# Performance work log

Measured on AMD Instinct MI355X. Metric: run time of the kernel, lower is better.

## Reference

```python
import jax, jax.numpy as jnp
import numpy as np

B, Q, K, DIM, H = 16, 256, 4096, 1024, 16
HD = DIM // H          # head_dim = 64
SCALE = float(np.sqrt(HD))
MAX_QUERIES = 64       # keep_first=True -> kept Q' = MAX_QUERIES + 1


def setup_inputs() -> dict:
    key = jax.random.key(0)
    ks = jax.random.split(key, 8)
    s = 1.0 / np.sqrt(DIM)
    return {
        "q": jax.random.normal(ks[0], (B, Q, DIM), jnp.float32),
        "k": jax.random.normal(ks[1], (B, K, DIM), jnp.float32),
        "v": jax.random.normal(ks[2], (B, K, DIM), jnp.float32),
        "Wq": jax.random.normal(ks[3], (DIM, DIM), jnp.float32) * s,
        "Wk": jax.random.normal(ks[4], (DIM, DIM), jnp.float32) * s,
        "Wv": jax.random.normal(ks[5], (DIM, DIM), jnp.float32) * s,
        "Wo": jax.random.normal(ks[6], (DIM, DIM), jnp.float32) * s,
        "bo": jnp.zeros((DIM,), jnp.float32),
    }


def _split_heads(x):  # [B, L, DIM] -> [B, L, H, HD]
    return x.reshape(x.shape[0], x.shape[1], H, HD)


def reference(q, k, v, Wq, Wk, Wv, Wo, bo):
    # QKV projections (no bias, matching qkv_bias=False; torch Linear is x @ W.T)
    qh = _split_heads(q @ Wq.T)   # [B,Q,H,HD]
    kh = _split_heads(k @ Wk.T)   # [B,K,H,HD]
    vh = _split_heads(v @ Wv.T)   # [B,K,H,HD]

    dots = jnp.einsum("bqhc,bkhc->bhqk", qh / SCALE, kh)  # [B,H,Q,K]

    # select_queries with keep_first=True: stats on detached dots over queries 1:
    sg = jax.lax.stop_gradient(dots)[:, :, 1:, :]          # [B,H,Q-1,K]
    stats = jax.nn.softmax(sg, axis=-2)                    # softmax over query axis
    score = stats.max(axis=(1, 3))                         # amax over (H, K) -> [B, Q-1]
    _, idx = jax.lax.top_k(score, MAX_QUERIES)             # [B, MAX_QUERIES]
    keep = jnp.concatenate(
        [jnp.zeros((dots.shape[0], 1), idx.dtype), idx + 1], axis=-1
    )                                                      # [B, Q'] with Q' = MAX_QUERIES+1

    dots_sel = jnp.take_along_axis(dots, keep[:, None, :, None], axis=2)  # [B,H,Q',K]

    # Competitive softmax: normalize over the (kept) query axis
    attn = jax.nn.softmax(dots_sel, axis=2)                # [B,H,Q',K]

    out = jnp.einsum("bhqk,bkhc->bqhc", attn, vh)          # [B,Q',H,HD]
    out = out.reshape(out.shape[0], out.shape[1], DIM)     # [B,Q',DIM]
    out = out @ Wo.T + bo
    return out, keep
```

## Files before the change

kernel.cpp:

```cpp
#include <hip/hip_runtime.h>
#include <hip/hip_bf16.h>
#include <math.h>

#define B_ 16
#define Q_ 256
#define K_ 4096
#define DIM_ 1024
#define H_ 16
#define HD_ 64
#define MQ_ 64
#define QP_ 65
#define SCALE_INV 0.125f

typedef unsigned short u16;
typedef __attribute__((ext_vector_type(8))) short bf16x8;
typedef __attribute__((ext_vector_type(4))) float f32x4;

__device__ __forceinline__ u16 f2bf_rne(float f) {
  unsigned u = __float_as_uint(f);
  u += 0x7fffu + ((u >> 16) & 1u);
  return (u16)(u >> 16);
}
__device__ __forceinline__ float bf2f(u16 h) {
  return __uint_as_float(((unsigned)h) << 16);
}
__device__ __forceinline__ void gload16(const void* g, void* l) {
  __builtin_amdgcn_global_load_lds(
      (const __attribute__((address_space(1))) unsigned int*)g,
      (__attribute__((address_space(3))) unsigned int*)l, 16, 0, 0);
}

__global__ __launch_bounds__(256) void split_bf16(
    const float* __restrict__ x, u16* __restrict__ hi, u16* __restrict__ lo,
    long n8, int wlo) {
  long i = (long)blockIdx.x * 256 + threadIdx.x;
  const long stride = (long)gridDim.x * 256;
  for (; i < n8; i += stride) {
    const float4 a = ((const float4*)x)[2 * i];
    const float4 b = ((const float4*)x)[2 * i + 1];
    const float xs[8] = {a.x, a.y, a.z, a.w, b.x, b.y, b.z, b.w};
    u16 h[8], l[8];
#pragma unroll
    for (int j = 0; j < 8; ++j) {
      h[j] = f2bf_rne(xs[j]);
      l[j] = f2bf_rne(xs[j] - bf2f(h[j]));
    }
    uint4 hv;
    hv.x = h[0] | ((unsigned)h[1] << 16);
    hv.y = h[2] | ((unsigned)h[3] << 16);
    hv.z = h[4] | ((unsigned)h[5] << 16);
    hv.w = h[6] | ((unsigned)h[7] << 16);
    ((uint4*)hi)[i] = hv;
    if (wlo) {
      uint4 lv;
      lv.x = l[0] | ((unsigned)l[1] << 16);
      lv.y = l[2] | ((unsigned)l[3] << 16);
      lv.z = l[4] | ((unsigned)l[5] << 16);
      lv.w = l[6] | ((unsigned)l[7] << 16);
      ((uint4*)lo)[i] = lv;
    }
  }
}

template <int NPROD, int OUTM>
__global__ __launch_bounds__(256) void mfma_gemm(
    const u16* __restrict__ Ahp, const u16* __restrict__ Alp,
    const u16* __restrict__ Bhp, const u16* __restrict__ Blp,
    float* __restrict__ C, u16* __restrict__ Cb) {
  __shared__ u16 Ah_s[128 * 32];
  __shared__ u16 Bh_s[128 * 32];
  __shared__ u16 Al_s[128 * 32];
  __shared__ u16 Bl_s[128 * 32];
  const int t = threadIdx.x;
  const int wave = t >> 6;
  const int lane = t & 63;
  const int wr = wave >> 1;
  const int wc = wave & 1;
  const int n0 = blockIdx.x * 128;
  const int m0 = blockIdx.y * 128;

  const int sr0 = wave * 32 + (lane >> 2);
  const int sr1 = sr0 + 16;
  const int sw0 = ((sr0 ^ (sr0 >> 2)) & 3) ^ (lane & 3);
  const int sw1 = ((sr1 ^ (sr1 >> 2)) & 3) ^ (lane & 3);
  const size_t gA0 = (size_t)(m0 + sr0) * DIM_ + sw0 * 8;
  const size_t gA1 = (size_t)(m0 + sr1) * DIM_ + sw1 * 8;
  const size_t gB0 = (size_t)(n0 + sr0) * DIM_ + sw0 * 8;
  const size_t gB1 = (size_t)(n0 + sr1) * DIM_ + sw1 * 8;
  u16* const lA0 = &Ah_s[(wave * 32) * 32];
  u16* const lA1 = &Ah_s[(wave * 32 + 16) * 32];
  u16* const lB0 = &Bh_s[(wave * 32) * 32];
  u16* const lB1 = &Bh_s[(wave * 32 + 16) * 32];
  u16* const lAl0 = &Al_s[(wave * 32) * 32];
  u16* const lAl1 = &Al_s[(wave * 32 + 16) * 32];
  u16* const lBl0 = &Bl_s[(wave * 32) * 32];
  u16* const lBl1 = &Bl_s[(wave * 32 + 16) * 32];

  int aoff[4], boff[4];
#pragma unroll
  for (int m = 0; m < 4; ++m) {
    const int r = wr * 64 + m * 16 + (lane & 15);
    const int p = ((r ^ (r >> 2)) & 3) ^ (lane >> 4);
    aoff[m] = r * 32 + p * 8;
  }
#pragma unroll
  for (int n = 0; n < 4; ++n) {
    const int r = wc * 64 + n * 16 + (lane & 15);
    const int p = ((r ^ (r >> 2)) & 3) ^ (lane >> 4);
    boff[n] = r * 32 + p * 8;
  }

  f32x4 acc[4][4];
#pragma unroll
  for (int m = 0; m < 4; ++m)
#pragma unroll
    for (int n = 0; n < 4; ++n) acc[m][n] = (f32x4)(0.f);

  for (int k0 = 0; k0 < DIM_; k0 += 32) {
    gload16(Ahp + gA0 + k0, lA0);
    gload16(Ahp + gA1 + k0, lA1);
    gload16(Bhp + gB0 + k0, lB0);
    gload16(Bhp + gB1 + k0, lB1);
    if (NPROD == 3) {
      gload16(Alp + gA0 + k0, lAl0);
      gload16(Alp + gA1 + k0, lAl1);
      gload16(Blp + gB0 + k0, lBl0);
      gload16(Blp + gB1 + k0, lBl1);
    }
    __syncthreads();
    {
      bf16x8 af[4], bfr[4];
#pragma unroll
      for (int m = 0; m < 4; ++m) af[m] = *(const bf16x8*)&Ah_s[aoff[m]];
#pragma unroll
      for (int n = 0; n < 4; ++n) bfr[n] = *(const bf16x8*)&Bh_s[boff[n]];
#pragma unroll
      for (int m = 0; m < 4; ++m)
#pragma unroll
        for (int n = 0; n < 4; ++n)
          acc[m][n] = __builtin_amdgcn_mfma_f32_16x16x32_bf16(
              af[m], bfr[n], acc[m][n], 0, 0, 0);
      if (NPROD == 3) {
#pragma unroll
        for (int n = 0; n < 4; ++n) bfr[n] = *(const bf16x8*)&Bl_s[boff[n]];
#pragma unroll
        for (int m = 0; m < 4; ++m)
#pragma unroll
          for (int n = 0; n < 4; ++n)
            acc[m][n] = __builtin_amdgcn_mfma_f32_16x16x32_bf16(
                af[m], bfr[n], acc[m][n], 0, 0, 0);
#pragma unroll
        for (int m = 0; m < 4; ++m) af[m] = *(const bf16x8*)&Al_s[aoff[m]];
#pragma unroll
        for (int n = 0; n < 4; ++n) bfr[n] = *(const bf16x8*)&Bh_s[boff[n]];
#pragma unroll
        for (int m = 0; m < 4; ++m)
#pragma unroll
          for (int n = 0; n < 4; ++n)
            acc[m][n] = __builtin_amdgcn_mfma_f32_16x16x32_bf16(
                af[m], bfr[n], acc[m][n], 0, 0, 0);
      }
    }
    __syncthreads();
  }
#pragma unroll
  for (int m = 0; m < 4; ++m) {
    const int row = m0 + wr * 64 + m * 16 + (lane >> 4) * 4;
#pragma unroll
    for (int n = 0; n < 4; ++n) {
      const int col = n0 + wc * 64 + n * 16 + (lane & 15);
#pragma unroll
      for (int j = 0; j < 4; ++j) {
        if (OUTM & 1) C[(size_t)(row + j) * DIM_ + col] = acc[m][n][j];
        if (OUTM & 2) Cb[(size_t)(row + j) * DIM_ + col] = f2bf_rne(acc[m][n][j]);
      }
    }
  }
}

#define GM 128
#define GN 128
#define GK 16

__global__ __launch_bounds__(256) void gemm_nt(
    const float* __restrict__ A, const float* __restrict__ W,
    float* __restrict__ C, int M, const float* __restrict__ bias) {
  __shared__ float As[GK][GM + 4];
  __shared__ float Ws[GK][GN + 4];
  const int t = threadIdx.x;
  const int m0 = blockIdx.x * GM;
  const int n0 = blockIdx.y * GN;
  const int lrow = t >> 2;
  const int lq = (t & 3) * 4;
  const int tm = (t >> 4) * 8;
  const int tn = (t & 15) * 8;
  float acc[8][8];
#pragma unroll
  for (int i = 0; i < 8; ++i)
#pragma unroll
    for (int j = 0; j < 8; ++j) acc[i][j] = 0.f;

  for (int k0 = 0; k0 < DIM_; k0 += GK) {
#pragma unroll
    for (int half = 0; half < 2; ++half) {
      const int row = lrow + half * 64;
      const int gm = m0 + row;
      float4 av = make_float4(0.f, 0.f, 0.f, 0.f);
      if (gm < M) av = *(const float4*)&A[(size_t)gm * DIM_ + k0 + lq];
      As[lq + 0][row] = av.x; As[lq + 1][row] = av.y;
      As[lq + 2][row] = av.z; As[lq + 3][row] = av.w;
      const int gn = n0 + row;
      const float4 wv = *(const float4*)&W[(size_t)gn * DIM_ + k0 + lq];
      Ws[lq + 0][row] = wv.x; Ws[lq + 1][row] = wv.y;
      Ws[lq + 2][row] = wv.z; Ws[lq + 3][row] = wv.w;
    }
    __syncthreads();
#pragma unroll
    for (int kk = 0; kk < GK; ++kk) {
      float a[8], bb[8];
      *(float4*)&a[0] = *(const float4*)&As[kk][tm];
      *(float4*)&a[4] = *(const float4*)&As[kk][tm + 4];
      *(float4*)&bb[0] = *(const float4*)&Ws[kk][tn];
      *(float4*)&bb[4] = *(const float4*)&Ws[kk][tn + 4];
#pragma unroll
      for (int i = 0; i < 8; ++i)
#pragma unroll
        for (int j = 0; j < 8; ++j)
          acc[i][j] = fmaf(a[i], bb[j], acc[i][j]);
    }
    __syncthreads();
  }
#pragma unroll
  for (int i = 0; i < 8; ++i) {
    const int gm = m0 + tm + i;
    if (gm < M) {
#pragma unroll
      for (int j = 0; j < 8; j += 4) {
        const int gn = n0 + tn + j;
        float4 ov;
        ov.x = acc[i][j + 0]; ov.y = acc[i][j + 1];
        ov.z = acc[i][j + 2]; ov.w = acc[i][j + 3];
        if (bias) {
          ov.x += bias[gn + 0]; ov.y += bias[gn + 1];
          ov.z += bias[gn + 2]; ov.w += bias[gn + 3];
        }
        *(float4*)&C[(size_t)gm * DIM_ + gn] = ov;
      }
    }
  }
}

#define KT 64
#define DC 32
#define KSPLIT 8

__device__ __forceinline__ unsigned fflip(float x) {
  const unsigned u = __float_as_uint(x);
  return (u & 0x80000000u) ? ~u : (u | 0x80000000u);
}

__global__ __launch_bounds__(256) void pass_a(
    const float* __restrict__ qh, const float* __restrict__ kh,
    unsigned* __restrict__ sbuf) {
  __shared__ float qs[DC][Q_ + 4];
  __shared__ float ksm[DC][KT + 4];
  __shared__ float red[32][KT + 1];
  __shared__ float cmax[KT];
  __shared__ float clse[KT];
  const int blk = blockIdx.x;
  const int b = blk >> 7;
  const int h = (blk >> 3) & 15;
  const int ks0 = (blk & 7) * (K_ / KSPLIT);
  const int t = threadIdx.x;
  const int tq = t >> 3;
  const int tk = t & 7;
  float rmax[8];
#pragma unroll
  for (int i = 0; i < 8; ++i) rmax[i] = -3.4e38f;

  for (int k0 = ks0; k0 < ks0 + K_ / KSPLIT; k0 += KT) {
    float acc[8][8];
#pragma unroll
    for (int i = 0; i < 8; ++i)
#pragma unroll
      for (int j = 0; j < 8; ++j) acc[i][j] = 0.f;

    for (int dc = 0; dc < HD_; dc += DC) {
      {
        const float* src = &qh[((size_t)(b * Q_ + t)) * DIM_ + h * HD_ + dc];
#pragma unroll
        for (int u = 0; u < DC / 4; ++u) {
          const float4 vv = *(const float4*)&src[u * 4];
          qs[u * 4 + 0][t] = vv.x * SCALE_INV;
          qs[u * 4 + 1][t] = vv.y * SCALE_INV;
          qs[u * 4 + 2][t] = vv.z * SCALE_INV;
          qs[u * 4 + 3][t] = vv.w * SCALE_INV;
        }
      }
      {
        const int r = t >> 2;
        const int qd = (t & 3) * 8;
        const float* src =
            &kh[((size_t)(b * K_ + k0 + r)) * DIM_ + h * HD_ + dc + qd];
#pragma unroll
        for (int u = 0; u < 2; ++u) {
          const float4 vv = *(const float4*)&src[u * 4];
          ksm[qd + u * 4 + 0][r] = vv.x; ksm[qd + u * 4 + 1][r] = vv.y;
          ksm[qd + u * 4 + 2][r] = vv.z; ksm[qd + u * 4 + 3][r] = vv.w;
        }
      }
      __syncthreads();
#pragma unroll
      for (int d = 0; d < DC; ++d) {
        float a[8], bb[8];
        *(float4*)&a[0] = *(const float4*)&qs[d][tq * 8];
        *(float4*)&a[4] = *(const float4*)&qs[d][tq * 8 + 4];
        *(float4*)&bb[0] = *(const float4*)&ksm[d][tk * 8];
        *(float4*)&bb[4] = *(const float4*)&ksm[d][tk * 8 + 4];
#pragma unroll
        for (int i = 0; i < 8; ++i)
#pragma unroll
          for (int j = 0; j < 8; ++j)
            acc[i][j] = fmaf(a[i], bb[j], acc[i][j]);
      }
      __syncthreads();
    }
#pragma unroll
    for (int j = 0; j < 8; ++j) {
      float m = -3.4e38f;
#pragma unroll
      for (int i = 0; i < 8; ++i) {
        if (tq == 0 && i == 0) continue;
        m = fmaxf(m, acc[i][j]);
      }
      red[tq][tk * 8 + j] = m;
    }
    __syncthreads();
    if (t < KT) {
      float m = -3.4e38f;
      for (int g = 0; g < 32; ++g) m = fmaxf(m, red[g][t]);
      cmax[t] = m;
    }
    __syncthreads();
#pragma unroll
    for (int j = 0; j < 8; ++j) {
      const float m = cmax[tk * 8 + j];
      float s = 0.f;
#pragma unroll
      for (int i = 0; i < 8; ++i) {
        if (tq == 0 && i == 0) continue;
        s += __expf(acc[i][j] - m);
      }
      red[tq][tk * 8 + j] = s;
    }
    __syncthreads();
    if (t < KT) {
      float s = 0.f;
      for (int g = 0; g < 32; ++g) s += red[g][t];
      clse[t] = cmax[t] + logf(s);
    }
    __syncthreads();
#pragma unroll
    for (int i = 0; i < 8; ++i) {
      float v = -3.4e38f;
#pragma unroll
      for (int j = 0; j < 8; ++j) v = fmaxf(v, acc[i][j] - clse[tk * 8 + j]);
      v = fmaxf(v, __shfl_xor(v, 1, 64));
      v = fmaxf(v, __shfl_xor(v, 2, 64));
      v = fmaxf(v, __shfl_xor(v, 4, 64));
      rmax[i] = fmaxf(rmax[i], v);
    }
    __syncthreads();
  }
  if (tk == 0) {
#pragma unroll
    for (int i = 0; i < 8; ++i) {
      const int qi = tq * 8 + i;
      if (qi > 0) atomicMax(&sbuf[b * Q_ + qi], fflip(rmax[i]));
    }
  }
}

__global__ void topk_kernel(const unsigned* __restrict__ sbuf,
                            int* __restrict__ keep, float* __restrict__ keepf) {
  const int b = blockIdx.x;
  const int lane = threadIdx.x;
  unsigned long long pk[4];
#pragma unroll
  for (int j = 0; j < 4; ++j) {
    const int q = 1 + lane + 64 * j;
    if (q <= 255) {
      const unsigned s = sbuf[b * Q_ + q];
      pk[j] = (((unsigned long long)s) << 32) | (unsigned)(256 - q);
    } else {
      pk[j] = 0ull;
    }
  }
  if (lane == 0) { keep[b * QP_] = 0; keepf[b * QP_] = 0.f; }
  for (int it = 0; it < MQ_; ++it) {
    unsigned long long best = pk[0];
#pragma unroll
    for (int j = 1; j < 4; ++j) best = (pk[j] > best) ? pk[j] : best;
    for (int m = 1; m < 64; m <<= 1) {
      const unsigned long long o = __shfl_xor(best, m, 64);
      best = (o > best) ? o : best;
    }
    const int q = 256 - (int)(best & 0xffffffffu);
#pragma unroll
    for (int j = 0; j < 4; ++j)
      if (pk[j] == best) pk[j] = 0ull;
    if (lane == 0) {
      keep[b * QP_ + 1 + it] = q;
      keepf[b * QP_ + 1 + it] = (float)q;
    }
  }
}

#define PSPL 4

__global__ __launch_bounds__(256) void pass_b_mfma(
    const float* __restrict__ qh, const u16* __restrict__ khb,
    const u16* __restrict__ vhb, const int* __restrict__ keep,
    float* __restrict__ part) {
  __shared__ __align__(16) char SH[72960];
  u16* const Qs = (u16*)SH;
  u16* const Ks = (u16*)(SH + 11520);
  u16* const Vs = (u16*)(SH + 29952);
  u16* const Ps = (u16*)(SH + 47360);
  float* const osum = (float*)(SH + 11520);

  const int bx = blockIdx.x;
  const int b = bx >> 6;
  const int h = (bx >> 2) & 15;
  const int sp = bx & 3;
  const int t = threadIdx.x;
  const int w = t >> 6;
  const int l = t & 63;
  const int g = l >> 4;
  const int a15 = l & 15;

  for (int idx = t; idx < 80 * 8; idx += 256) {
    const int row = idx >> 3, ch = idx & 7;
    uint4 pk;
    if (row < QP_) {
      const int kq = keep[b * QP_ + row];
      const float* src = &qh[((size_t)(b * Q_ + kq)) * DIM_ + h * HD_ + ch * 8];
      const float4 x0 = *(const float4*)&src[0];
      const float4 x1 = *(const float4*)&src[4];
      pk.x = f2bf_rne(x0.x * SCALE_INV) | ((unsigned)f2bf_rne(x0.y * SCALE_INV) << 16);
      pk.y = f2bf_rne(x0.z * SCALE_INV) | ((unsigned)f2bf_rne(x0.w * SCALE_INV) << 16);
      pk.z = f2bf_rne(x1.x * SCALE_INV) | ((unsigned)f2bf_rne(x1.y * SCALE_INV) << 16);
      pk.w = f2bf_rne(x1.z * SCALE_INV) | ((unsigned)f2bf_rne(x1.w * SCALE_INV) << 16);
    } else {
      pk = make_uint4(0, 0, 0, 0);
    }
    *(uint4*)&Qs[row * 72 + ch * 8] = pk;
  }
  __syncthreads();

  f32x4 oacc[5][4];
#pragma unroll
  for (int mt = 0; mt < 5; ++mt)
#pragma unroll
    for (int dt = 0; dt < 4; ++dt) oacc[mt][dt] = (f32x4)(0.f);

  const int kt0 = sp * (K_ / PSPL);
  for (int kt = 0; kt < K_ / PSPL; kt += 128) {
    const int k0 = kt0 + kt;
    uint4 kreg[4], vreg[4];
    int srow[4], sch[4];
#pragma unroll
    for (int s = 0; s < 4; ++s) {
      const int c = t + 256 * s;
      srow[s] = c >> 3;
      sch[s] = c & 7;
      const size_t gidx =
          ((size_t)(b * K_ + k0 + srow[s])) * DIM_ + h * HD_ + sch[s] * 8;
      kreg[s] = *(const uint4*)&khb[gidx];
      vreg[s] = *(const uint4*)&vhb[gidx];
    }
    __syncthreads();
#pragma unroll
    for (int s = 0; s < 4; ++s) {
      *(uint4*)&Ks[srow[s] * 72 + sch[s] * 8] = kreg[s];
      uint2 v0; v0.x = vreg[s].x; v0.y = vreg[s].y;
      uint2 v1; v1.x = vreg[s].z; v1.y = vreg[s].w;
      *(uint2*)&Vs[srow[s] * 68 + sch[s] * 8] = v0;
      *(uint2*)&Vs[srow[s] * 68 + sch[s] * 8 + 4] = v1;
    }
    __syncthreads();

    f32x4 S[5][2];
#pragma unroll
    for (int mt = 0; mt < 5; ++mt)
#pragma unroll
      for (int nt = 0; nt < 2; ++nt) S[mt][nt] = (f32x4)(0.f);
#pragma unroll
    for (int kk = 0; kk < 2; ++kk) {
      bf16x8 aq[5];
#pragma unroll
      for (int mt = 0; mt < 5; ++mt)
        aq[mt] = *(const bf16x8*)&Qs[(mt * 16 + a15) * 72 + kk * 32 + g * 8];
#pragma unroll
      for (int nt = 0; nt < 2; ++nt) {
        const bf16x8 bk =
            *(const bf16x8*)&Ks[(w * 32 + nt * 16 + a15) * 72 + kk * 32 + g * 8];
#pragma unroll
        for (int mt = 0; mt < 5; ++mt)
          S[mt][nt] = __builtin_amdgcn_mfma_f32_16x16x32_bf16(aq[mt], bk,
                                                              S[mt][nt], 0, 0, 0);
      }
    }
#pragma unroll
    for (int nt = 0; nt < 2; ++nt) {
      float m = -3.4e38f;
#pragma unroll
      for (int mt = 0; mt < 5; ++mt)
#pragma unroll
        for (int j = 0; j < 4; ++j) {
          const bool valid = (mt < 4) | ((g == 0) & (j == 0));
          if (valid) m = fmaxf(m, S[mt][nt][j]);
        }
      m = fmaxf(m, __shfl_xor(m, 16, 64));
      m = fmaxf(m, __shfl_xor(m, 32, 64));
      float s = 0.f;
#pragma unroll
      for (int mt = 0; mt < 5; ++mt)
#pragma unroll
        for (int j = 0; j < 4; ++j) {
          const bool valid = (mt < 4) | ((g == 0) & (j == 0));
          const float p = valid ? __expf(S[mt][nt][j] - m) : 0.f;
          S[mt][nt][j] = p;
          s += p;
        }
      s += __shfl_xor(s, 16, 64);
      s += __shfl_xor(s, 32, 64);
      const float r = 1.f / s;
#pragma unroll
      for (int mt = 0; mt < 5; ++mt)
#pragma unroll
        for (int j = 0; j < 4; ++j)
          Ps[w * 3200 + (mt * 16 + g * 4 + j) * 40 + nt * 16 + a15] =
              f2bf_rne(S[mt][nt][j] * r);
    }
    bf16x8 ap[5];
#pragma unroll
    for (int mt = 0; mt < 5; ++mt)
      ap[mt] = *(const bf16x8*)&Ps[w * 3200 + (mt * 16 + a15) * 40 + g * 8];
#pragma unroll
    for (int dt = 0; dt < 4; ++dt) {
      bf16x8 bv;
#pragma unroll
      for (int e = 0; e < 8; ++e)
        bv[e] = (short)Vs[(w * 32 + g * 8 + e) * 68 + dt * 16 + a15];
#pragma unroll
      for (int mt = 0; mt < 5; ++mt)
        oacc[mt][dt] = __builtin_amdgcn_mfma_f32_16x16x32_bf16(ap[mt], bv,
                                                               oacc[mt][dt], 0, 0, 0);
    }
  }

#pragma unroll
  for (int dt = 0; dt < 4; ++dt) {
    __syncthreads();
#pragma unroll
    for (int mt = 0; mt < 5; ++mt)
#pragma unroll
      for (int j = 0; j < 4; ++j)
        osum[w * 1360 + (mt * 16 + g * 4 + j) * 17 + a15] = oacc[mt][dt][j];
    __syncthreads();
    for (int idx = t; idx < QP_ * 16; idx += 256) {
      const int q = idx >> 4, c = idx & 15;
      const float sm = osum[q * 17 + c] + osum[1360 + q * 17 + c] +
                       osum[2720 + q * 17 + c] + osum[4080 + q * 17 + c];
      part[(((size_t)sp * B_ + b) * QP_ + q) * DIM_ + h * 64 + dt * 16 + c] = sm;
    }
  }
}

__global__ __launch_bounds__(256) void pass_b(
    const float* __restrict__ qh, const float* __restrict__ kh,
    const float* __restrict__ vh, const int* __restrict__ keep,
    float* __restrict__ part) {
  __shared__ float qs[QP_][HD_ + 4];
  __shared__ float kv[KT][HD_ + 4];
  __shared__ float att[QP_][KT + 4];
  __shared__ float cmax[KT];
  __shared__ float crcp[KT];
  const int bx = blockIdx.x;
  const int b = bx >> 6;
  const int h = (bx >> 2) & 15;
  const int sp = bx & 3;
  const int t = threadIdx.x;

  if (t < QP_) {
    const int kq = keep[b * QP_ + t];
    const float* src = &qh[((size_t)(b * Q_ + kq)) * DIM_ + h * HD_];
#pragma unroll
    for (int u = 0; u < HD_ / 4; ++u) {
      float4 vv = *(const float4*)&src[u * 4];
      vv.x *= SCALE_INV; vv.y *= SCALE_INV;
      vv.z *= SCALE_INV; vv.w *= SCALE_INV;
      *(float4*)&qs[t][u * 4] = vv;
    }
  }
  const int c = t & 63;
  const int jg = t >> 6;
  const int j0 = jg * 17;
  const int j1 = (jg == 3) ? QP_ : (j0 + 17);
  const int j2 = t >> 2;
  const int cg = (t & 3) * 16;
  const int r = t >> 2;
  const int qd = (t & 3) * 16;
  float oacc[16], oacc2[16];
#pragma unroll
  for (int u = 0; u < 16; ++u) { oacc[u] = 0.f; oacc2[u] = 0.f; }

  __syncthreads();

  const int kbeg = sp * (K_ / PSPL);
  const int kend = kbeg + K_ / PSPL;
  for (int k0 = kbeg; k0 < kend; k0 += KT) {
    {
      const float* src = &kh[((size_t)(b * K_ + k0 + r)) * DIM_ + h * HD_ + qd];
#pragma unroll
      for (int u = 0; u < 4; ++u)
        *(float4*)&kv[r][qd + u * 4] = *(const float4*)&src[u * 4];
    }
    __syncthreads();
    {
      float4 kr[16];
#pragma unroll
      for (int u = 0; u < 16; ++u) kr[u] = *(const float4*)&kv[c][u * 4];
      for (int j = j0; j < j1; ++j) {
        float4 s4 = make_float4(0.f, 0.f, 0.f, 0.f);
#pragma unroll
        for (int u = 0; u < 16; ++u) {
          const float4 qv = *(const float4*)&qs[j][u * 4];
          s4.x = fmaf(qv.x, kr[u].x, s4.x);
          s4.y = fmaf(qv.y, kr[u].y, s4.y);
          s4.z = fmaf(qv.z, kr[u].z, s4.z);
          s4.w = fmaf(qv.w, kr[u].w, s4.w);
        }
        att[j][c] = (s4.x + s4.y) + (s4.z + s4.w);
      }
    }
    __syncthreads();
    {
      const float* src = &vh[((size_t)(b * K_ + k0 + r)) * DIM_ + h * HD_ + qd];
#pragma unroll
      for (int u = 0; u < 4; ++u)
        *(float4*)&kv[r][qd + u * 4] = *(const float4*)&src[u * 4];
      if (t < KT) {
        float m = att[0][t];
        for (int j = 1; j < QP_; ++j) m = fmaxf(m, att[j][t]);
        float s = 0.f;
        for (int j = 0; j < QP_; ++j) s += __expf(att[j][t] - m);
        cmax[t] = m;
        crcp[t] = 1.f / s;
      }
    }
    __syncthreads();
    for (int e = t; e < QP_ * KT; e += 256) {
      const int jj = e >> 6;
      const int cc = e & 63;
      att[jj][cc] = __expf(att[jj][cc] - cmax[cc]) * crcp[cc];
    }
    __syncthreads();
    {
      for (int ck = 0; ck < KT; ++ck) {
        const float a = att[j2][ck];
#pragma unroll
        for (int u = 0; u < 4; ++u) {
          const float4 vv = *(const float4*)&kv[ck][cg + u * 4];
          oacc[u * 4 + 0] = fmaf(a, vv.x, oacc[u * 4 + 0]);
          oacc[u * 4 + 1] = fmaf(a, vv.y, oacc[u * 4 + 1]);
          oacc[u * 4 + 2] = fmaf(a, vv.z, oacc[u * 4 + 2]);
          oacc[u * 4 + 3] = fmaf(a, vv.w, oacc[u * 4 + 3]);
        }
      }
      if (t < 4) {
        const int cg2 = t * 16;
        for (int ck = 0; ck < KT; ++ck) {
          const float a = att[64][ck];
#pragma unroll
          for (int u = 0; u < 4; ++u) {
            const float4 vv = *(const float4*)&kv[ck][cg2 + u * 4];
            oacc2[u * 4 + 0] = fmaf(a, vv.x, oacc2[u * 4 + 0]);
            oacc2[u * 4 + 1] = fmaf(a, vv.y, oacc2[u * 4 + 1]);
            oacc2[u * 4 + 2] = fmaf(a, vv.z, oacc2[u * 4 + 2]);
            oacc2[u * 4 + 3] = fmaf(a, vv.w, oacc2[u * 4 + 3]);
          }
        }
      }
    }
    __syncthreads();
  }
  {
    float* dst =
        &part[(((size_t)sp * B_ + b) * QP_ + j2) * DIM_ + h * HD_ + cg];
    *(float4*)&dst[0] = make_float4(oacc[0], oacc[1], oacc[2], oacc[3]);
    *(float4*)&dst[4] = make_float4(oacc[4], oacc[5], oacc[6], oacc[7]);
    *(float4*)&dst[8] = make_float4(oacc[8], oacc[9], oacc[10], oacc[11]);
    *(float4*)&dst[12] = make_float4(oacc[12], oacc[13], oacc[14], oacc[15]);
    if (t < 4) {
      float* dst2 =
          &part[(((size_t)sp * B_ + b) * QP_ + 64) * DIM_ + h * HD_ + t * 16];
      *(float4*)&dst2[0] = make_float4(oacc2[0], oacc2[1], oacc2[2], oacc2[3]);
      *(float4*)&dst2[4] = make_float4(oacc2[4], oacc2[5], oacc2[6], oacc2[7]);
      *(float4*)&dst2[8] = make_float4(oacc2[8], oacc2[9], oacc2[10], oacc2[11]);
      *(float4*)&dst2[12] = make_float4(oacc2[12], oacc2[13], oacc2[14], oacc2[15]);
    }
  }
}

__global__ __launch_bounds__(256) void reduce_part(
    const float* __restrict__ part, float* __restrict__ opre) {
  const long n4 = (long)B_ * QP_ * DIM_ / 4;
  const long i = (long)blockIdx.x * 256 + threadIdx.x;
  if (i >= n4) return;
  float4 s = ((const float4*)part)[i];
#pragma unroll
  for (int sp = 1; sp < PSPL; ++sp) {
    const float4 p = ((const float4*)part)[(long)sp * n4 + i];
    s.x += p.x; s.y += p.y; s.z += p.z; s.w += p.w;
  }
  ((float4*)opre)[i] = s;
}

extern "C" void kernel_launch(void* const* d_in, const int* in_sizes, int n_in,
                              void* d_out, int out_size, void* d_ws, size_t ws_size,
                              hipStream_t stream) {
  const float* q  = (const float*)d_in[0];
  const float* k  = (const float*)d_in[1];
  const float* v  = (const float*)d_in[2];
  const float* Wq = (const float*)d_in[3];
  const float* Wk = (const float*)d_in[4];
  const float* Wv = (const float*)d_in[5];
  const float* Wo = (const float*)d_in[6];
  const float* bo = (const float*)d_in[7];
  float* out = (float*)d_out;

  char* base = (char*)d_ws;
  size_t off = 0;
  auto alloc = [&](size_t bytes) {
    char* p = base + off;
    off = (off + bytes + 255) & ~(size_t)255;
    return (void*)p;
  };
  float* qh   = (float*)alloc((size_t)B_ * Q_ * DIM_ * 4);
  float* kh   = (float*)alloc((size_t)B_ * K_ * DIM_ * 4);
  float* opre = (float*)alloc((size_t)B_ * QP_ * DIM_ * 4);
  unsigned* sbuf = (unsigned*)alloc((size_t)B_ * Q_ * 4);
  int* keep   = (int*)alloc((size_t)B_ * QP_ * 4);
  u16* kh_b = (u16*)alloc((size_t)B_ * K_ * DIM_ * 2);
  u16* vh_b = (u16*)alloc((size_t)B_ * K_ * DIM_ * 2);
  u16* kHi = (u16*)alloc((size_t)B_ * K_ * DIM_ * 2);
  u16* kLo = (u16*)alloc((size_t)B_ * K_ * DIM_ * 2);
  u16* wHi = (u16*)alloc((size_t)DIM_ * DIM_ * 2);
  u16* wLo = (u16*)alloc((size_t)DIM_ * DIM_ * 2);
  const bool big = (off <= ws_size);
  float* part = big ? (float*)kHi
                    : (float*)alloc((size_t)PSPL * B_ * QP_ * DIM_ * 4);
  float* vh_f = (float*)kh_b;
  float* keepf = out + (size_t)B_ * QP_ * DIM_;

  hipMemsetAsync(sbuf, 0, B_ * Q_ * sizeof(unsigned), stream);

  const dim3 blk(256);
  if (big) {
    const long nKV8 = (long)B_ * K_ * DIM_ / 8;
    const long nW8 = (long)DIM_ * DIM_ / 8;
    split_bf16<<<2048, blk, 0, stream>>>(k, kHi, kLo, nKV8, 1);
    split_bf16<<<512, blk, 0, stream>>>(Wk, wHi, wLo, nW8, 1);
    mfma_gemm<3, 3><<<dim3(DIM_ / 128, B_ * K_ / 128), blk, 0, stream>>>(
        kHi, kLo, wHi, wLo, kh, kh_b);
    split_bf16<<<2048, blk, 0, stream>>>(v, kHi, nullptr, nKV8, 0);
    split_bf16<<<512, blk, 0, stream>>>(Wv, wHi, nullptr, nW8, 0);
    mfma_gemm<1, 2><<<dim3(DIM_ / 128, B_ * K_ / 128), blk, 0, stream>>>(
        kHi, nullptr, wHi, nullptr, nullptr, vh_b);
  } else {
    gemm_nt<<<dim3(B_ * K_ / GM, DIM_ / GN), blk, 0, stream>>>(k, Wk, kh, B_ * K_, nullptr);
    gemm_nt<<<dim3(B_ * K_ / GM, DIM_ / GN), blk, 0, stream>>>(v, Wv, vh_f, B_ * K_, nullptr);
  }
  gemm_nt<<<dim3(B_ * Q_ / GM, DIM_ / GN), blk, 0, stream>>>(q, Wq, qh, B_ * Q_, nullptr);
  pass_a<<<dim3(B_ * H_ * KSPLIT), blk, 0, stream>>>(qh, kh, sbuf);
  topk_kernel<<<dim3(B_), dim3(64), 0, stream>>>(sbuf, keep, keepf);
  if (big) {
    pass_b_mfma<<<dim3(B_ * H_ * PSPL), blk, 0, stream>>>(qh, kh_b, vh_b, keep, part);
  } else {
    pass_b<<<dim3(B_ * H_ * PSPL), blk, 0, stream>>>(qh, kh, vh_f, keep, part);
  }
  reduce_part<<<dim3((B_ * QP_ * DIM_ / 4 + 255) / 256), blk, 0, stream>>>(part, opre);
  gemm_nt<<<dim3((B_ * QP_ + GM - 1) / GM, DIM_ / GN), blk, 0, stream>>>(
      opre, Wo, out, B_ * QP_, bo);
}
```

Measured before the change: 1.828 ms.

## Move query-selection scoring to split-fp16 MFMA and store K/V projections as fp16

The selection pass now runs on matrix cores with a three-product hi/lo fp16 split, replacing the fp32 scalar pass_a. To feed it, the K projection writes fp16 hi/lo halves instead of an fp32 tensor, and Q is split into fp16 hi/lo after its GEMM. The attention pass switches from bf16 to fp16 operands. This removes the fp32 kh write and read and puts the dominant QK^T scoring work on MFMA, at the cost of an extra split kernel and possible fp16 range/precision differences in the top-k selection.

```diff
diff --git a/kernel.cpp b/kernel.cpp
--- a/kernel.cpp
+++ b/kernel.cpp
@@ -14,6 +14,8 @@
 
 typedef unsigned short u16;
 typedef __attribute__((ext_vector_type(8))) short bf16x8;
+typedef __attribute__((ext_vector_type(8))) _Float16 f16x8;
+typedef __attribute__((ext_vector_type(8))) short s16x8;
 typedef __attribute__((ext_vector_type(4))) float f32x4;
 
 __device__ __forceinline__ u16 f2bf_rne(float f) {
@@ -23,6 +25,13 @@
 }
 __device__ __forceinline__ float bf2f(u16 h) {
   return __uint_as_float(((unsigned)h) << 16);
+}
+__device__ __forceinline__ u16 f2h_bits(float f) {
+  _Float16 h = (_Float16)f;
+  return *(u16*)&h;
+}
+__device__ __forceinline__ f16x8 as_f16x8(s16x8 v) {
+  return __builtin_bit_cast(f16x8, v);
 }
 __device__ __forceinline__ void gload16(const void* g, void* l) {
   __builtin_amdgcn_global_load_lds(
@@ -62,11 +71,43 @@
   }
 }
 
+__global__ __launch_bounds__(256) void split_f16(
+    const float* __restrict__ x, u16* __restrict__ hi, u16* __restrict__ lo,
+    long n8) {
+  long i = (long)blockIdx.x * 256 + threadIdx.x;
+  const long stride = (long)gridDim.x * 256;
+  for (; i < n8; i += stride) {
+    const float4 a = ((const float4*)x)[2 * i];
+    const float4 b = ((const float4*)x)[2 * i + 1];
+    const float xs[8] = {a.x, a.y, a.z, a.w, b.x, b.y, b.z, b.w};
+    u16 h[8], l[8];
+#pragma unroll
+    for (int j = 0; j < 8; ++j) {
+      _Float16 hh = (_Float16)xs[j];
+      _Float16 ll = (_Float16)(xs[j] - (float)hh);
+      h[j] = *(u16*)&hh;
+      l[j] = *(u16*)&ll;
+    }
+    uint4 hv;
+    hv.x = h[0] | ((unsigned)h[1] << 16);
+    hv.y = h[2] | ((unsigned)h[3] << 16);
+    hv.z = h[4] | ((unsigned)h[5] << 16);
+    hv.w = h[6] | ((unsigned)h[7] << 16);
+    ((uint4*)hi)[i] = hv;
+    uint4 lv;
+    lv.x = l[0] | ((unsigned)l[1] << 16);
+    lv.y = l[2] | ((unsigned)l[3] << 16);
+    lv.z = l[4] | ((unsigned)l[5] << 16);
+    lv.w = l[6] | ((unsigned)l[7] << 16);
+    ((uint4*)lo)[i] = lv;
+  }
+}
+
 template <int NPROD, int OUTM>
 __global__ __launch_bounds__(256) void mfma_gemm(
     const u16* __restrict__ Ahp, const u16* __restrict__ Alp,
     const u16* __restrict__ Bhp, const u16* __restrict__ Blp,
-    float* __restrict__ C, u16* __restrict__ Cb) {
+    float* __restrict__ C, u16* __restrict__ ChH, u16* __restrict__ ChL) {
   __shared__ u16 Ah_s[128 * 32];
   __shared__ u16 Bh_s[128 * 32];
   __shared__ u16 Al_s[128 * 32];
@@ -171,8 +212,17 @@
       const int col = n0 + wc * 64 + n * 16 + (lane & 15);
 #pragma unroll
       for (int j = 0; j < 4; ++j) {
-        if (OUTM & 1) C[(size_t)(row + j) * DIM_ + col] = acc[m][n][j];
-        if (OUTM & 2) Cb[(size_t)(row + j) * DIM_ + col] = f2bf_rne(acc[m][n][j]);
+        const size_t idx = (size_t)(row + j) * DIM_ + col;
+        const float a = acc[m][n][j];
+        if (OUTM & 1) C[idx] = a;
+        if (OUTM & 4) {
+          _Float16 hi = (_Float16)a;
+          ChH[idx] = *(u16*)&hi;
+          if (OUTM & 8) {
+            _Float16 lo = (_Float16)(a - (float)hi);
+            ChL[idx] = *(u16*)&lo;
+          }
+        }
       }
     }
   }
@@ -250,14 +300,177 @@
   }
 }
 
+__device__ __forceinline__ unsigned fflip(float x) {
+  const unsigned u = __float_as_uint(x);
+  return (u & 0x80000000u) ? ~u : (u | 0x80000000u);
+}
+
+#define AKT 64
+
+__global__ __launch_bounds__(256) void pass_a_mfma(
+    const u16* __restrict__ qhH, const u16* __restrict__ qhL,
+    const u16* __restrict__ khH, const u16* __restrict__ khL,
+    unsigned* __restrict__ sbuf) {
+  __shared__ u16 KsH[AKT * 72];
+  __shared__ u16 KsL[AKT * 72];
+  __shared__ float red[4][2 * AKT];
+  const int bx = blockIdx.x;
+  const int b = bx >> 7;
+  const int h = (bx >> 3) & 15;
+  const int ks0 = (bx & 7) * (K_ / 8);
+  const int t = threadIdx.x;
+  const int w = t >> 6;
+  const int l = t & 63;
+  const int g = l >> 4;
+  const int a15 = l & 15;
+
+  f16x8 qA[2][4][2];
+#pragma unroll
+  for (int mt = 0; mt < 4; ++mt) {
+    const int qrow = w * 64 + mt * 16 + a15;
+    const size_t base = ((size_t)(b * Q_ + qrow)) * DIM_ + h * HD_;
+#pragma unroll
+    for (int ks = 0; ks < 2; ++ks) {
+      qA[0][mt][ks] = *(const f16x8*)&qhH[base + ks * 32 + g * 8];
+      qA[1][mt][ks] = *(const f16x8*)&qhL[base + ks * 32 + g * 8];
+    }
+  }
+  float rmax[4][4];
+#pragma unroll
+  for (int mt = 0; mt < 4; ++mt)
+#pragma unroll
+    for (int j = 0; j < 4; ++j) rmax[mt][j] = -3.4e38f;
+
+  for (int k0 = ks0; k0 < ks0 + K_ / 8; k0 += AKT) {
+    uint4 sH[2], sL[2];
+    int sr[2], sc[2];
+#pragma unroll
+    for (int s = 0; s < 2; ++s) {
+      const int c = t + 256 * s;
+      sr[s] = c >> 3;
+      sc[s] = c & 7;
+      const size_t gidx =
+          ((size_t)(b * K_ + k0 + sr[s])) * DIM_ + h * HD_ + sc[s] * 8;
+      sH[s] = *(const uint4*)&khH[gidx];
+      sL[s] = *(const uint4*)&khL[gidx];
+    }
+    __syncthreads();
+#pragma unroll
+    for (int s = 0; s < 2; ++s) {
+      *(uint4*)&KsH[sr[s] * 72 + sc[s] * 8] = sH[s];
+      *(uint4*)&KsL[sr[s] * 72 + sc[s] * 8] = sL[s];
+    }
+    __syncthreads();
+
+    f32x4 acc[4][4];
+#pragma unroll
+    for (int mt = 0; mt < 4; ++mt)
+#pragma unroll
+      for (int kt = 0; kt < 4; ++kt) acc[mt][kt] = (f32x4)(0.f);
+#pragma unroll
+    for (int ks = 0; ks < 2; ++ks) {
+#pragma unroll
+      for (int kt = 0; kt < 4; ++kt) {
+        const f16x8 bH =
+            *(const f16x8*)&KsH[(kt * 16 + a15) * 72 + ks * 32 + g * 8];
+        const f16x8 bL =
+            *(const f16x8*)&KsL[(kt * 16 + a15) * 72 + ks * 32 + g * 8];
+#pragma unroll
+        for (int mt = 0; mt < 4; ++mt) {
+          acc[mt][kt] = __builtin_amdgcn_mfma_f32_16x16x32_f16(
+              qA[0][mt][ks], bH, acc[mt][kt], 0, 0, 0);
+          acc[mt][kt] = __builtin_amdgcn_mfma_f32_16x16x32_f16(
+              qA[0][mt][ks], bL, acc[mt][kt], 0, 0, 0);
+          acc[mt][kt] = __builtin_amdgcn_mfma_f32_16x16x32_f16(
+              qA[1][mt][ks], bH, acc[mt][kt], 0, 0, 0);
+        }
+      }
+    }
+#pragma unroll
+    for (int mt = 0; mt < 4; ++mt)
+#pragma unroll
+      for (int kt = 0; kt < 4; ++kt) acc[mt][kt] = acc[mt][kt] * 0.125f;
+
+    float cmax[4];
+#pragma unroll
+    for (int kt = 0; kt < 4; ++kt) {
+      float m = -3.4e38f;
+#pragma unroll
+      for (int mt = 0; mt < 4; ++mt)
+#pragma unroll
+        for (int j = 0; j < 4; ++j) {
+          const bool ex = (w == 0) & (mt == 0) & (g == 0) & (j == 0);
+          if (!ex) m = fmaxf(m, acc[mt][kt][j]);
+        }
+      m = fmaxf(m, __shfl_xor(m, 16, 64));
+      m = fmaxf(m, __shfl_xor(m, 32, 64));
+      cmax[kt] = m;
+    }
+    if (l < 16) {
+#pragma unroll
+      for (int kt = 0; kt < 4; ++kt) red[w][kt * 16 + l] = cmax[kt];
+    }
+    __syncthreads();
+#pragma unroll
+    for (int kt = 0; kt < 4; ++kt)
+      cmax[kt] = fmaxf(fmaxf(red[0][kt * 16 + a15], red[1][kt * 16 + a15]),
+                       fmaxf(red[2][kt * 16 + a15], red[3][kt * 16 + a15]));
+    float csum[4];
+#pragma unroll
+    for (int kt = 0; kt < 4; ++kt) {
+      float s = 0.f;
+#pragma unroll
+      for (int mt = 0; mt < 4; ++mt)
+#pragma unroll
+        for (int j = 0; j < 4; ++j) {
+          const bool ex = (w == 0) & (mt == 0) & (g == 0) & (j == 0);
+          if (!ex) s += __expf(acc[mt][kt][j] - cmax[kt]);
+        }
+      s += __shfl_xor(s, 16, 64);
+      s += __shfl_xor(s, 32, 64);
+      csum[kt] = s;
+    }
+    if (l < 16) {
+#pragma unroll
+      for (int kt = 0; kt < 4; ++kt) red[w][AKT + kt * 16 + l] = csum[kt];
+    }
+    __syncthreads();
+    float lse[4];
+#pragma unroll
+    for (int kt = 0; kt < 4; ++kt) {
+      const float s = red[0][AKT + kt * 16 + a15] + red[1][AKT + kt * 16 + a15] +
+                      red[2][AKT + kt * 16 + a15] + red[3][AKT + kt * 16 + a15];
+      lse[kt] = cmax[kt] + logf(s);
+    }
+#pragma unroll
+    for (int mt = 0; mt < 4; ++mt)
+#pragma unroll
+      for (int j = 0; j < 4; ++j) {
+        float v = -3.4e38f;
+#pragma unroll
+        for (int kt = 0; kt < 4; ++kt)
+          v = fmaxf(v, acc[mt][kt][j] - lse[kt]);
+        v = fmaxf(v, __shfl_xor(v, 1, 64));
+        v = fmaxf(v, __shfl_xor(v, 2, 64));
+        v = fmaxf(v, __shfl_xor(v, 4, 64));
+        v = fmaxf(v, __shfl_xor(v, 8, 64));
+        rmax[mt][j] = fmaxf(rmax[mt][j], v);
+      }
+  }
+  if (a15 == 0) {
+#pragma unroll
+    for (int mt = 0; mt < 4; ++mt)
+#pragma unroll
+      for (int j = 0; j < 4; ++j) {
+        const int qi = w * 64 + mt * 16 + g * 4 + j;
+        if (qi > 0) atomicMax(&sbuf[b * Q_ + qi], fflip(rmax[mt][j]));
+      }
+  }
+}
+
 #define KT 64
 #define DC 32
 #define KSPLIT 8
-
-__device__ __forceinline__ unsigned fflip(float x) {
-  const unsigned u = __float_as_uint(x);
-  return (u & 0x80000000u) ? ~u : (u | 0x80000000u);
-}
 
 __global__ __launch_bounds__(256) void pass_a(
     const float* __restrict__ qh, const float* __restrict__ kh,
@@ -447,10 +660,10 @@
       const float* src = &qh[((size_t)(b * Q_ + kq)) * DIM_ + h * HD_ + ch * 8];
       const float4 x0 = *(const float4*)&src[0];
       const float4 x1 = *(const float4*)&src[4];
-      pk.x = f2bf_rne(x0.x * SCALE_INV) | ((unsigned)f2bf_rne(x0.y * SCALE_INV) << 16);
-      pk.y = f2bf_rne(x0.z * SCALE_INV) | ((unsigned)f2bf_rne(x0.w * SCALE_INV) << 16);
-      pk.z = f2bf_rne(x1.x * SCALE_INV) | ((unsigned)f2bf_rne(x1.y * SCALE_INV) << 16);
-      pk.w = f2bf_rne(x1.z * SCALE_INV) | ((unsigned)f2bf_rne(x1.w * SCALE_INV) << 16);
+      pk.x = f2h_bits(x0.x * SCALE_INV) | ((unsigned)f2h_bits(x0.y * SCALE_INV) << 16);
+      pk.y = f2h_bits(x0.z * SCALE_INV) | ((unsigned)f2h_bits(x0.w * SCALE_INV) << 16);
+      pk.z = f2h_bits(x1.x * SCALE_INV) | ((unsigned)f2h_bits(x1.y * SCALE_INV) << 16);
+      pk.w = f2h_bits(x1.z * SCALE_INV) | ((unsigned)f2h_bits(x1.w * SCALE_INV) << 16);
     } else {
       pk = make_uint4(0, 0, 0, 0);
     }
@@ -497,18 +710,18 @@
       for (int nt = 0; nt < 2; ++nt) S[mt][nt] = (f32x4)(0.f);
 #pragma unroll
     for (int kk = 0; kk < 2; ++kk) {
-      bf16x8 aq[5];
+      f16x8 aq[5];
 #pragma unroll
       for (int mt = 0; mt < 5; ++mt)
-        aq[mt] = *(const bf16x8*)&Qs[(mt * 16 + a15) * 72 + kk * 32 + g * 8];
+        aq[mt] = *(const f16x8*)&Qs[(mt * 16 + a15) * 72 + kk * 32 + g * 8];
 #pragma unroll
       for (int nt = 0; nt < 2; ++nt) {
-        const bf16x8 bk =
-            *(const bf16x8*)&Ks[(w * 32 + nt * 16 + a15) * 72 + kk * 32 + g * 8];
+        const f16x8 bk =
+            *(const f16x8*)&Ks[(w * 32 + nt * 16 + a15) * 72 + kk * 32 + g * 8];
 #pragma unroll
         for (int mt = 0; mt < 5; ++mt)
-          S[mt][nt] = __builtin_amdgcn_mfma_f32_16x16x32_bf16(aq[mt], bk,
-                                                              S[mt][nt], 0, 0, 0);
+          S[mt][nt] = __builtin_amdgcn_mfma_f32_16x16x32_f16(aq[mt], bk,
+                                                             S[mt][nt], 0, 0, 0);
       }
     }
 #pragma unroll
@@ -541,22 +754,22 @@
 #pragma unroll
         for (int j = 0; j < 4; ++j)
           Ps[w * 3200 + (mt * 16 + g * 4 + j) * 40 + nt * 16 + a15] =
-              f2bf_rne(S[mt][nt][j] * r);
-    }
-    bf16x8 ap[5];
+              f2h_bits(S[mt][nt][j] * r);
+    }
+    f16x8 ap[5];
 #pragma unroll
     for (int mt = 0; mt < 5; ++mt)
-      ap[mt] = *(const bf16x8*)&Ps[w * 3200 + (mt * 16 + a15) * 40 + g * 8];
+      ap[mt] = *(const f16x8*)&Ps[w * 3200 + (mt * 16 + a15) * 40 + g * 8];
 #pragma unroll
     for (int dt = 0; dt < 4; ++dt) {
-      bf16x8 bv;
+      s16x8 bv;
 #pragma unroll
       for (int e = 0; e < 8; ++e)
         bv[e] = (short)Vs[(w * 32 + g * 8 + e) * 68 + dt * 16 + a15];
 #pragma unroll
       for (int mt = 0; mt < 5; ++mt)
-        oacc[mt][dt] = __builtin_amdgcn_mfma_f32_16x16x32_bf16(ap[mt], bv,
-                                                               oacc[mt][dt], 0, 0, 0);
+        oacc[mt][dt] = __builtin_amdgcn_mfma_f32_16x16x32_f16(
+            ap[mt], as_f16x8(bv), oacc[mt][dt], 0, 0, 0);
     }
   }
 
@@ -749,49 +962,60 @@
     return (void*)p;
   };
   float* qh   = (float*)alloc((size_t)B_ * Q_ * DIM_ * 4);
-  float* kh   = (float*)alloc((size_t)B_ * K_ * DIM_ * 4);
   float* opre = (float*)alloc((size_t)B_ * QP_ * DIM_ * 4);
   unsigned* sbuf = (unsigned*)alloc((size_t)B_ * Q_ * 4);
   int* keep   = (int*)alloc((size_t)B_ * QP_ * 4);
-  u16* kh_b = (u16*)alloc((size_t)B_ * K_ * DIM_ * 2);
-  u16* vh_b = (u16*)alloc((size_t)B_ * K_ * DIM_ * 2);
+  const size_t common_off = off;
+  u16* qhH = (u16*)alloc((size_t)B_ * Q_ * DIM_ * 2);
+  u16* qhL = (u16*)alloc((size_t)B_ * Q_ * DIM_ * 2);
+  u16* khH = (u16*)alloc((size_t)B_ * K_ * DIM_ * 2);
+  u16* khL = (u16*)alloc((size_t)B_ * K_ * DIM_ * 2);
+  u16* vhH = (u16*)alloc((size_t)B_ * K_ * DIM_ * 2);
   u16* kHi = (u16*)alloc((size_t)B_ * K_ * DIM_ * 2);
   u16* kLo = (u16*)alloc((size_t)B_ * K_ * DIM_ * 2);
   u16* wHi = (u16*)alloc((size_t)DIM_ * DIM_ * 2);
   u16* wLo = (u16*)alloc((size_t)DIM_ * DIM_ * 2);
   const bool big = (off <= ws_size);
-  float* part = big ? (float*)kHi
-                    : (float*)alloc((size_t)PSPL * B_ * QP_ * DIM_ * 4);
-  float* vh_f = (float*)kh_b;
   float* keepf = out + (size_t)B_ * QP_ * DIM_;
+  const dim3 blk(256);
 
   hipMemsetAsync(sbuf, 0, B_ * Q_ * sizeof(unsigned), stream);
 
-  const dim3 blk(256);
   if (big) {
+    float* part = (float*)kHi;
     const long nKV8 = (long)B_ * K_ * DIM_ / 8;
     const long nW8 = (long)DIM_ * DIM_ / 8;
+    const long nQ8 = (long)B_ * Q_ * DIM_ / 8;
     split_bf16<<<2048, blk, 0, stream>>>(k, kHi, kLo, nKV8, 1);
     split_bf16<<<512, blk, 0, stream>>>(Wk, wHi, wLo, nW8, 1);
-    mfma_gemm<3, 3><<<dim3(DIM_ / 128, B_ * K_ / 128), blk, 0, stream>>>(
-        kHi, kLo, wHi, wLo, kh, kh_b);
+    mfma_gemm<3, 12><<<dim3(DIM_ / 128, B_ * K_ / 128), blk, 0, stream>>>(
+        kHi, kLo, wHi, wLo, nullptr, khH, khL);
     split_bf16<<<2048, blk, 0, stream>>>(v, kHi, nullptr, nKV8, 0);
     split_bf16<<<512, blk, 0, stream>>>(Wv, wHi, nullptr, nW8, 0);
-    mfma_gemm<1, 2><<<dim3(DIM_ / 128, B_ * K_ / 128), blk, 0, stream>>>(
-        kHi, nullptr, wHi, nullptr, nullptr, vh_b);
+    mfma_gemm<1, 4><<<dim3(DIM_ / 128, B_ * K_ / 128), blk, 0, stream>>>(
+        kHi, nullptr, wHi, nullptr, nullptr, vhH, nullptr);
+    gemm_nt<<<dim3(B_ * Q_ / GM, DIM_ / GN), blk, 0, stream>>>(
+        q, Wq, qh, B_ * Q_, nullptr);
+    split_f16<<<512, blk, 0, stream>>>(qh, qhH, qhL, nQ8);
+    pass_a_mfma<<<dim3(B_ * H_ * 8), blk, 0, stream>>>(qhH, qhL, khH, khL, sbuf);
+    topk_kernel<<<dim3(B_), dim3(64), 0, stream>>>(sbuf, keep, keepf);
+    pass_b_mfma<<<dim3(B_ * H_ * PSPL), blk, 0, stream>>>(qh, khH, vhH, keep, part);
+    reduce_part<<<dim3((B_ * QP_ * DIM_ / 4 + 255) / 256), blk, 0, stream>>>(part, opre);
+    gemm_nt<<<dim3((B_ * QP_ + GM - 1) / GM, DIM_ / GN), blk, 0, stream>>>(
+        opre, Wo, out, B_ * QP_, bo);
   } else {
+    off = common_off;
+    float* kh = (float*)alloc((size_t)B_ * K_ * DIM_ * 4);
+    float* vh = (float*)alloc((size_t)B_ * K_ * DIM_ * 4);
+    float* part = (float*)alloc((size_t)PSPL * B_ * QP_ * DIM_ * 4);
     gemm_nt<<<dim3(B_ * K_ / GM, DIM_ / GN), blk, 0, stream>>>(k, Wk, kh, B_ * K_, nullptr);
-    gemm_nt<<<dim3(B_ * K_ / GM, DIM_ / GN), blk, 0, stream>>>(v, Wv, vh_f, B_ * K_, nullptr);
-  }
-  gemm_nt<<<dim3(B_ * Q_ / GM, DIM_ / GN), blk, 0, stream>>>(q, Wq, qh, B_ * Q_, nullptr);
-  pass_a<<<dim3(B_ * H_ * KSPLIT), blk, 0, stream>>>(qh, kh, sbuf);
-  topk_kernel<<<dim3(B_), dim3(64), 0, stream>>>(sbuf, keep, keepf);
-  if (big) {
-    pass_b_mfma<<<dim3(B_ * H_ * PSPL), blk, 0, stream>>>(qh, kh_b, vh_b, keep, part);
-  } else {
-    pass_b<<<dim3(B_ * H_ * PSPL), blk, 0, stream>>>(qh, kh, vh_f, keep, part);
-  }
-  reduce_part<<<dim3((B_ * QP_ * DIM_ / 4 + 255) / 256), blk, 0, stream>>>(part, opre);
-  gemm_nt<<<dim3((B_ * QP_ + GM - 1) / GM, DIM_ / GN), blk, 0, stream>>>(
-      opre, Wo, out, B_ * QP_, bo);
-}
+    gemm_nt<<<dim3(B_ * K_ / GM, DIM_ / GN), blk, 0, stream>>>(v, Wv, vh, B_ * K_, nullptr);
+    gemm_nt<<<dim3(B_ * Q_ / GM, DIM_ / GN), blk, 0, stream>>>(q, Wq, qh, B_ * Q_, nullptr);
+    pass_a<<<dim3(B_ * H_ * KSPLIT), blk, 0, stream>>>(qh, kh, sbuf);
+    topk_kernel<<<dim3(B_), dim3(64), 0, stream>>>(sbuf, keep, keepf);
+    pass_b<<<dim3(B_ * H_ * PSPL), blk, 0, stream>>>(qh, kh, vh, keep, part);
+    reduce_part<<<dim3((B_ * QP_ * DIM_ / 4 + 255) / 256), blk, 0, stream>>>(part, opre);
+    gemm_nt<<<dim3((B_ * QP_ + GM - 1) / GM, DIM_ / GN), blk, 0, stream>>>(
+        opre, Wo, out, B_ * QP_, bo);
+  }
+}
```

Measured after the change: 1.512 ms. 17.3% less time.
